# Kernel tuning notes

Hardware: AMD Instinct MI355X
Metric: run time of the kernel (lower is better)

The kernel has to match this reference:

```python
import jax, jax.numpy as jnp
import numpy as np


def setup_inputs() -> dict:
    key = jax.random.key(0)
    k1, k2 = jax.random.split(key)
    B, EMB, CODES, NUM_TOKENS = 16, 64, 16384, 1024
    x_in = jax.random.normal(k1, (B, EMB, CODES), dtype=jnp.float32)
    code_embedding = jax.random.uniform(k2, (NUM_TOKENS, EMB), dtype=jnp.float32)
    return {"x_in": x_in, "code_embedding": code_embedding}


def reference(x_in, code_embedding):
    # x_in: [B, emb, codes]; code_embedding: [num_tokens, emb]
    x_t = jnp.transpose(x_in, (0, 2, 1))  # [B, codes, emb]
    # squared euclidean distances (argmin is invariant to sqrt used by cdist)
    x2 = jnp.sum(x_t * x_t, axis=-1)                      # [B, codes]
    e2 = jnp.sum(code_embedding * code_embedding, axis=-1)  # [num_tokens]
    dots = jnp.einsum('bce,ke->bck', x_t, code_embedding)   # [B, codes, num_tokens]
    dist2 = x2[:, :, None] - 2.0 * dots + e2[None, None, :]
    indices = jnp.argmin(dist2, axis=2)                   # [B, codes]
    x_out = jnp.transpose(code_embedding[indices], (0, 2, 1))  # [B, emb, codes]
    return x_out, indices[:, :, None]  # indices keepdim like torch argmin(keepdim=True)
```

## Files before the change

### kernel.cpp

```cpp
#include <hip/hip_runtime.h>


#define BB 16
#define EMB 64
#define CODES 16384
#define NT 1024
#define NTILES 64

typedef __attribute__((ext_vector_type(8))) short s16x8;
typedef __attribute__((ext_vector_type(4))) float f32x4;
typedef __attribute__((ext_vector_type(4))) int i32x4;
typedef unsigned int u32;

__device__ inline short bf16_hi(float f) { return (short)(__builtin_bit_cast(u32, f) >> 16); }
__device__ inline float hi_part(float f) { return __builtin_bit_cast(float, __builtin_bit_cast(u32, f) & 0xFFFF0000u); }
__device__ inline u32 umin_(u32 a, u32 b) { return a < b ? a : b; }
__device__ inline u32 umax_(u32 a, u32 b) { return a > b ? a : b; }

#define WSE_OFF   0
#define WSH_OFF   266240
#define WSH2_OFF  270336

__global__ __launch_bounds__(256) void vq_prep(const float* __restrict__ E,
                                               char* __restrict__ wsE,
                                               float* __restrict__ wsh,
                                               float* __restrict__ wsh2) {
  const int bid = blockIdx.x, tid = threadIdx.x;
  if (bid < 32) {
    const int gid = bid * 256 + tid;
    const int nt = gid >> 7, ks = (gid >> 6) & 1, lane = gid & 63;
    const int col = lane & 15, quad = lane >> 4;
    const int n = nt * 16 + col;
    const int k0 = ks * 32 + quad * 8;
    const float* ep = E + n * EMB + k0;
    s16x8 hv, lv;
    #pragma unroll
    for (int j = 0; j < 8; ++j) {
      float v = ep[j];
      float hf = hi_part(v);
      hv[j] = bf16_hi(v);
      lv[j] = bf16_hi(v - hf);
    }
    char* base = wsE + ((size_t)nt << 12) + ((size_t)ks << 10) + lane * 16;
    *(i32x4*)(base)        = __builtin_bit_cast(i32x4, hv);
    *(i32x4*)(base + 2048) = __builtin_bit_cast(i32x4, lv);
  } else {
    const int n = (bid - 32) * 256 + tid;
    if (n < NT) {
      const float4* ep = (const float4*)(E + n * EMB);
      float s = 0.f;
      #pragma unroll
      for (int g = 0; g < 16; ++g) { float4 v = ep[g]; s += v.x*v.x + v.y*v.y + v.z*v.z + v.w*v.w; }
      const float h = -0.5f * s;
      wsh[n] = h;
      wsh2[n] = 16384.f * (h + 128.f);
    }
  }
}

__global__ __launch_bounds__(64, 2) void vq_main(
    const float* __restrict__ x, const float* __restrict__ E,
    const char* __restrict__ wsE, const float* __restrict__ wsh,
    const float* __restrict__ wsh2,
    float* __restrict__ xout, float* __restrict__ iout) {
  __shared__ uint2 cand[64];
  const int lane = threadIdx.x;
  const int col = lane & 15, quad = lane >> 4;
  const int b = blockIdx.y;
  const int c0 = blockIdx.x * 64;

  s16x8 ah[4][2], al[4][2];
  #pragma unroll
  for (int mt = 0; mt < 4; ++mt) {
    #pragma unroll
    for (int ks = 0; ks < 2; ++ks) {
      s16x8 hv, lv;
      #pragma unroll
      for (int j = 0; j < 8; ++j) {
        const int e = ks * 32 + quad * 8 + j;
        float v = x[((size_t)b * EMB + e) * CODES + (size_t)(c0 + mt * 16 + col)] * 16384.f;
        float hf = hi_part(v);
        hv[j] = bf16_hi(v);
        lv[j] = bf16_hi(v - hf);
      }
      ah[mt][ks] = hv;
      al[mt][ks] = lv;
    }
  }

  u32 k1[4][4], k2[4][4];
  #pragma unroll
  for (int mt = 0; mt < 4; ++mt)
    #pragma unroll
    for (int r = 0; r < 4; ++r) { k1[mt][r] = 0u; k2[mt][r] = 0u; }

  u32 inv = 1023u - (u32)col;
  const char* p = wsE + lane * 16;
  const float* hp = wsh2 + col;

  i32x4 nb0 = *(const i32x4*)(p);
  i32x4 nb1 = *(const i32x4*)(p + 1024);
  i32x4 nb2 = *(const i32x4*)(p + 2048);
  i32x4 nb3 = *(const i32x4*)(p + 3072);
  float nch = *hp;

  #pragma unroll 4
  for (int nt = 0; nt < NTILES; ++nt) {
    const s16x8 bh0 = __builtin_bit_cast(s16x8, nb0);
    const s16x8 bh1 = __builtin_bit_cast(s16x8, nb1);
    const s16x8 bl0 = __builtin_bit_cast(s16x8, nb2);
    const s16x8 bl1 = __builtin_bit_cast(s16x8, nb3);
    const float ch = nch;

    p += 4096; hp += 16;
    nb0 = *(const i32x4*)(p);
    nb1 = *(const i32x4*)(p + 1024);
    nb2 = *(const i32x4*)(p + 2048);
    nb3 = *(const i32x4*)(p + 3072);
    nch = *hp;

    f32x4 acc[4];
    #pragma unroll
    for (int mt = 0; mt < 4; ++mt) {
      acc[mt] = (f32x4){ch, ch, ch, ch};
      acc[mt] = __builtin_amdgcn_mfma_f32_16x16x32_bf16(ah[mt][0], bh0, acc[mt], 0, 0, 0);
      acc[mt] = __builtin_amdgcn_mfma_f32_16x16x32_bf16(ah[mt][1], bh1, acc[mt], 0, 0, 0);
      acc[mt] = __builtin_amdgcn_mfma_f32_16x16x32_bf16(al[mt][0], bh0, acc[mt], 0, 0, 0);
      acc[mt] = __builtin_amdgcn_mfma_f32_16x16x32_bf16(al[mt][1], bh1, acc[mt], 0, 0, 0);
      acc[mt] = __builtin_amdgcn_mfma_f32_16x16x32_bf16(ah[mt][0], bl0, acc[mt], 0, 0, 0);
      acc[mt] = __builtin_amdgcn_mfma_f32_16x16x32_bf16(ah[mt][1], bl1, acc[mt], 0, 0, 0);
    }

    #pragma unroll
    for (int mt = 0; mt < 4; ++mt) {
      #pragma unroll
      for (int r = 0; r < 4; ++r) {
        u32 q = (u32)acc[mt][r];
        u32 key = (q << 10) + inv;
        u32 t = umin_(key, k1[mt][r]);
        k1[mt][r] = umax_(key, k1[mt][r]);
        k2[mt][r] = umax_(t, k2[mt][r]);
      }
    }
    inv -= 16u;
  }

  #pragma unroll
  for (int mt = 0; mt < 4; ++mt) {
    #pragma unroll
    for (int r = 0; r < 4; ++r) {
      u32 a1 = k1[mt][r], a2 = k2[mt][r];
      #pragma unroll
      for (int m = 1; m <= 8; m <<= 1) {
        u32 r1 = __shfl_xor(a1, m, 64);
        u32 r2 = __shfl_xor(a2, m, 64);
        u32 t = umin_(a1, r1);
        a1 = umax_(a1, r1);
        a2 = umax_(umax_(a2, r2), t);
      }
      if (col == r) cand[mt * 16 + quad * 4 + r] = make_uint2(a1, a2);
    }
  }
  __syncthreads();

  const u32 K1 = cand[lane].x, K2 = cand[lane].y;
  const int i1 = 1023 - (int)(K1 & 1023u);
  const int i2 = 1023 - (int)(K2 & 1023u);
  const float* xq = x + (size_t)b * EMB * CODES + (size_t)(c0 + lane);
  const float4* e1 = (const float4*)(E + i1 * EMB);
  const float4* e2 = (const float4*)(E + i2 * EMB);
  float d10 = 0, d11 = 0, d12 = 0, d13 = 0, d20 = 0, d21 = 0, d22 = 0, d23 = 0;
  #pragma unroll
  for (int g = 0; g < 16; ++g) {
    float4 a = e1[g], c4 = e2[g];
    float x0 = xq[(size_t)(4 * g + 0) * CODES];
    float x1 = xq[(size_t)(4 * g + 1) * CODES];
    float x2 = xq[(size_t)(4 * g + 2) * CODES];
    float x3 = xq[(size_t)(4 * g + 3) * CODES];
    d10 = fmaf(x0, a.x, d10);  d11 = fmaf(x1, a.y, d11);
    d12 = fmaf(x2, a.z, d12);  d13 = fmaf(x3, a.w, d13);
    d20 = fmaf(x0, c4.x, d20); d21 = fmaf(x1, c4.y, d21);
    d22 = fmaf(x2, c4.z, d22); d23 = fmaf(x3, c4.w, d23);
  }
  const float s1 = ((d10 + d11) + (d12 + d13)) + wsh[i1];
  const float s2 = ((d20 + d21) + (d22 + d23)) + wsh[i2];
  const bool take2 = (s2 > s1) || (s2 == s1 && i2 < i1);
  const int idx = take2 ? i2 : i1;

  const float* Er = E + idx * EMB;
  float* xo = xout + (size_t)b * EMB * CODES + (size_t)(c0 + lane);
  #pragma unroll
  for (int e = 0; e < EMB; ++e) xo[(size_t)e * CODES] = Er[e];
  iout[(size_t)b * CODES + (size_t)(c0 + lane)] = (float)idx;
}

extern "C" void kernel_launch(void* const* d_in, const int* in_sizes, int n_in,
                              void* d_out, int out_size, void* d_ws, size_t ws_size,
                              hipStream_t stream) {
  const float* x = (const float*)d_in[0];
  const float* E = (const float*)d_in[1];
  float* xout = (float*)d_out;
  float* iout = (float*)d_out + (size_t)BB * EMB * CODES;

  char* wsE  = (char*)d_ws + WSE_OFF;
  float* wsh  = (float*)((char*)d_ws + WSH_OFF);
  float* wsh2 = (float*)((char*)d_ws + WSH2_OFF);

  vq_prep<<<36, 256, 0, stream>>>(E, wsE, wsh, wsh2);
  vq_main<<<dim3(CODES / 64, BB), 64, 0, stream>>>(x, E, wsE, wsh, wsh2, xout, iout);
}
```

Before: 225.8 us.

## Stage codebook tiles in double-buffered LDS shared by four waves per block

Blocks grow from one wave covering 64 codes to four waves covering 128 codes, each wave now holding 32 codes. The bf16 hi/lo codebook is loaded cooperatively into double-buffered shared memory in chunks of four tiles, so every wave reuses one staged copy instead of streaming the whole codebook from global memory itself. The final gather and write-out is spread across all 256 threads. The cost is fewer MFMA tiles per wave per codebook fetch, more LDS reads, and a block barrier after every chunk.

```diff
diff --git a/kernel.cpp b/kernel.cpp
--- a/kernel.cpp
+++ b/kernel.cpp
@@ -6,6 +6,8 @@
 #define CODES 16384
 #define NT 1024
 #define NTILES 64
+#define CHUNK 4
+#define EPOCHS (NTILES / CHUNK)
 
 typedef __attribute__((ext_vector_type(8))) short s16x8;
 typedef __attribute__((ext_vector_type(4))) float f32x4;
@@ -58,27 +60,29 @@
   }
 }
 
-__global__ __launch_bounds__(64, 2) void vq_main(
+__global__ __launch_bounds__(256, 5) void vq_main(
     const float* __restrict__ x, const float* __restrict__ E,
     const char* __restrict__ wsE, const float* __restrict__ wsh,
     const float* __restrict__ wsh2,
     float* __restrict__ xout, float* __restrict__ iout) {
-  __shared__ uint2 cand[64];
-  const int lane = threadIdx.x;
+  __shared__ char smem[2 * CHUNK * 4096];
+  const int tid = threadIdx.x;
+  const int wave = tid >> 6, lane = tid & 63;
   const int col = lane & 15, quad = lane >> 4;
   const int b = blockIdx.y;
-  const int c0 = blockIdx.x * 64;
-
-  s16x8 ah[4][2], al[4][2];
+  const int c0 = blockIdx.x * 128;
+  const int cw = c0 + wave * 32;
+
+  s16x8 ah[2][2], al[2][2];
   #pragma unroll
-  for (int mt = 0; mt < 4; ++mt) {
+  for (int mt = 0; mt < 2; ++mt) {
     #pragma unroll
     for (int ks = 0; ks < 2; ++ks) {
       s16x8 hv, lv;
       #pragma unroll
       for (int j = 0; j < 8; ++j) {
         const int e = ks * 32 + quad * 8 + j;
-        float v = x[((size_t)b * EMB + e) * CODES + (size_t)(c0 + mt * 16 + col)] * 16384.f;
+        float v = x[((size_t)b * EMB + e) * CODES + (size_t)(cw + mt * 16 + col)] * 16384.f;
         float hf = hi_part(v);
         hv[j] = bf16_hi(v);
         lv[j] = bf16_hi(v - hf);
@@ -88,65 +92,91 @@
     }
   }
 
-  u32 k1[4][4], k2[4][4];
+  u32 k1[2][4], k2[2][4];
   #pragma unroll
-  for (int mt = 0; mt < 4; ++mt)
+  for (int mt = 0; mt < 2; ++mt)
     #pragma unroll
     for (int r = 0; r < 4; ++r) { k1[mt][r] = 0u; k2[mt][r] = 0u; }
 
   u32 inv = 1023u - (u32)col;
-  const char* p = wsE + lane * 16;
   const float* hp = wsh2 + col;
 
-  i32x4 nb0 = *(const i32x4*)(p);
-  i32x4 nb1 = *(const i32x4*)(p + 1024);
-  i32x4 nb2 = *(const i32x4*)(p + 2048);
-  i32x4 nb3 = *(const i32x4*)(p + 3072);
-  float nch = *hp;
-
-  #pragma unroll 4
-  for (int nt = 0; nt < NTILES; ++nt) {
-    const s16x8 bh0 = __builtin_bit_cast(s16x8, nb0);
-    const s16x8 bh1 = __builtin_bit_cast(s16x8, nb1);
-    const s16x8 bl0 = __builtin_bit_cast(s16x8, nb2);
-    const s16x8 bl1 = __builtin_bit_cast(s16x8, nb3);
-    const float ch = nch;
-
-    p += 4096; hp += 16;
-    nb0 = *(const i32x4*)(p);
-    nb1 = *(const i32x4*)(p + 1024);
-    nb2 = *(const i32x4*)(p + 2048);
-    nb3 = *(const i32x4*)(p + 3072);
-    nch = *hp;
-
-    f32x4 acc[4];
-    #pragma unroll
-    for (int mt = 0; mt < 4; ++mt) {
-      acc[mt] = (f32x4){ch, ch, ch, ch};
-      acc[mt] = __builtin_amdgcn_mfma_f32_16x16x32_bf16(ah[mt][0], bh0, acc[mt], 0, 0, 0);
-      acc[mt] = __builtin_amdgcn_mfma_f32_16x16x32_bf16(ah[mt][1], bh1, acc[mt], 0, 0, 0);
-      acc[mt] = __builtin_amdgcn_mfma_f32_16x16x32_bf16(al[mt][0], bh0, acc[mt], 0, 0, 0);
-      acc[mt] = __builtin_amdgcn_mfma_f32_16x16x32_bf16(al[mt][1], bh1, acc[mt], 0, 0, 0);
-      acc[mt] = __builtin_amdgcn_mfma_f32_16x16x32_bf16(ah[mt][0], bl0, acc[mt], 0, 0, 0);
-      acc[mt] = __builtin_amdgcn_mfma_f32_16x16x32_bf16(ah[mt][1], bl1, acc[mt], 0, 0, 0);
-    }
-
-    #pragma unroll
-    for (int mt = 0; mt < 4; ++mt) {
-      #pragma unroll
-      for (int r = 0; r < 4; ++r) {
-        u32 q = (u32)acc[mt][r];
-        u32 key = (q << 10) + inv;
-        u32 t = umin_(key, k1[mt][r]);
-        k1[mt][r] = umax_(key, k1[mt][r]);
-        k2[mt][r] = umax_(t, k2[mt][r]);
-      }
-    }
-    inv -= 16u;
-  }
-
+  const char* gbase = wsE + wave * 4096 + lane * 16;
+  i32x4 st0, st1, st2, st3;
+  {
+    const char* g = gbase;
+    st0 = *(const i32x4*)(g);
+    st1 = *(const i32x4*)(g + 1024);
+    st2 = *(const i32x4*)(g + 2048);
+    st3 = *(const i32x4*)(g + 3072);
+    char* d = smem + wave * 4096 + lane * 16;
+    *(i32x4*)(d)        = st0;
+    *(i32x4*)(d + 1024) = st1;
+    *(i32x4*)(d + 2048) = st2;
+    *(i32x4*)(d + 3072) = st3;
+  }
+  __syncthreads();
+
+  for (int c = 0; c < EPOCHS; ++c) {
+    const char* rb = smem + (c & 1) * (CHUNK * 4096) + lane * 16;
+    char* wb = smem + ((c + 1) & 1) * (CHUNK * 4096) + wave * 4096 + lane * 16;
+
+    if (c < EPOCHS - 1) {
+      const char* g = gbase + (size_t)(c + 1) * (CHUNK * 4096);
+      st0 = *(const i32x4*)(g);
+      st1 = *(const i32x4*)(g + 1024);
+      st2 = *(const i32x4*)(g + 2048);
+      st3 = *(const i32x4*)(g + 3072);
+    }
+
+    #pragma unroll
+    for (int t = 0; t < CHUNK; ++t) {
+      const char* p = rb + t * 4096;
+      const s16x8 bh0 = __builtin_bit_cast(s16x8, *(const i32x4*)(p));
+      const s16x8 bh1 = __builtin_bit_cast(s16x8, *(const i32x4*)(p + 1024));
+      const s16x8 bl0 = __builtin_bit_cast(s16x8, *(const i32x4*)(p + 2048));
+      const s16x8 bl1 = __builtin_bit_cast(s16x8, *(const i32x4*)(p + 3072));
+      const float ch = hp[(c * CHUNK + t) * 16];
+
+      f32x4 acc[2];
+      #pragma unroll
+      for (int mt = 0; mt < 2; ++mt) {
+        acc[mt] = (f32x4){ch, ch, ch, ch};
+        acc[mt] = __builtin_amdgcn_mfma_f32_16x16x32_bf16(ah[mt][0], bh0, acc[mt], 0, 0, 0);
+        acc[mt] = __builtin_amdgcn_mfma_f32_16x16x32_bf16(ah[mt][1], bh1, acc[mt], 0, 0, 0);
+        acc[mt] = __builtin_amdgcn_mfma_f32_16x16x32_bf16(al[mt][0], bh0, acc[mt], 0, 0, 0);
+        acc[mt] = __builtin_amdgcn_mfma_f32_16x16x32_bf16(al[mt][1], bh1, acc[mt], 0, 0, 0);
+        acc[mt] = __builtin_amdgcn_mfma_f32_16x16x32_bf16(ah[mt][0], bl0, acc[mt], 0, 0, 0);
+        acc[mt] = __builtin_amdgcn_mfma_f32_16x16x32_bf16(ah[mt][1], bl1, acc[mt], 0, 0, 0);
+      }
+
+      #pragma unroll
+      for (int mt = 0; mt < 2; ++mt) {
+        #pragma unroll
+        for (int r = 0; r < 4; ++r) {
+          u32 q = (u32)acc[mt][r];
+          u32 key = (q << 10) + inv;
+          u32 tt = umin_(key, k1[mt][r]);
+          k1[mt][r] = umax_(key, k1[mt][r]);
+          k2[mt][r] = umax_(tt, k2[mt][r]);
+        }
+      }
+      inv -= 16u;
+    }
+
+    if (c < EPOCHS - 1) {
+      *(i32x4*)(wb)        = st0;
+      *(i32x4*)(wb + 1024) = st1;
+      *(i32x4*)(wb + 2048) = st2;
+      *(i32x4*)(wb + 3072) = st3;
+    }
+    __syncthreads();
+  }
+
+  uint2* cand = (uint2*)smem;
+  int* idxs = (int*)(smem + 1024);
   #pragma unroll
-  for (int mt = 0; mt < 4; ++mt) {
+  for (int mt = 0; mt < 2; ++mt) {
     #pragma unroll
     for (int r = 0; r < 4; ++r) {
       u32 a1 = k1[mt][r], a2 = k2[mt][r];
@@ -158,40 +188,49 @@
         a1 = umax_(a1, r1);
         a2 = umax_(umax_(a2, r2), t);
       }
-      if (col == r) cand[mt * 16 + quad * 4 + r] = make_uint2(a1, a2);
+      if (col == r) cand[wave * 32 + mt * 16 + quad * 4 + r] = make_uint2(a1, a2);
     }
   }
   __syncthreads();
 
-  const u32 K1 = cand[lane].x, K2 = cand[lane].y;
-  const int i1 = 1023 - (int)(K1 & 1023u);
-  const int i2 = 1023 - (int)(K2 & 1023u);
-  const float* xq = x + (size_t)b * EMB * CODES + (size_t)(c0 + lane);
-  const float4* e1 = (const float4*)(E + i1 * EMB);
-  const float4* e2 = (const float4*)(E + i2 * EMB);
-  float d10 = 0, d11 = 0, d12 = 0, d13 = 0, d20 = 0, d21 = 0, d22 = 0, d23 = 0;
-  #pragma unroll
-  for (int g = 0; g < 16; ++g) {
-    float4 a = e1[g], c4 = e2[g];
-    float x0 = xq[(size_t)(4 * g + 0) * CODES];
-    float x1 = xq[(size_t)(4 * g + 1) * CODES];
-    float x2 = xq[(size_t)(4 * g + 2) * CODES];
-    float x3 = xq[(size_t)(4 * g + 3) * CODES];
-    d10 = fmaf(x0, a.x, d10);  d11 = fmaf(x1, a.y, d11);
-    d12 = fmaf(x2, a.z, d12);  d13 = fmaf(x3, a.w, d13);
-    d20 = fmaf(x0, c4.x, d20); d21 = fmaf(x1, c4.y, d21);
-    d22 = fmaf(x2, c4.z, d22); d23 = fmaf(x3, c4.w, d23);
-  }
-  const float s1 = ((d10 + d11) + (d12 + d13)) + wsh[i1];
-  const float s2 = ((d20 + d21) + (d22 + d23)) + wsh[i2];
-  const bool take2 = (s2 > s1) || (s2 == s1 && i2 < i1);
-  const int idx = take2 ? i2 : i1;
-
-  const float* Er = E + idx * EMB;
-  float* xo = xout + (size_t)b * EMB * CODES + (size_t)(c0 + lane);
-  #pragma unroll
-  for (int e = 0; e < EMB; ++e) xo[(size_t)e * CODES] = Er[e];
-  iout[(size_t)b * CODES + (size_t)(c0 + lane)] = (float)idx;
+  if (tid < 128) {
+    const u32 K1 = cand[tid].x, K2 = cand[tid].y;
+    const int i1 = 1023 - (int)(K1 & 1023u);
+    const int i2 = 1023 - (int)(K2 & 1023u);
+    const float* xq = x + (size_t)b * EMB * CODES + (size_t)(c0 + tid);
+    const float4* e1 = (const float4*)(E + i1 * EMB);
+    const float4* e2 = (const float4*)(E + i2 * EMB);
+    float d10 = 0, d11 = 0, d12 = 0, d13 = 0, d20 = 0, d21 = 0, d22 = 0, d23 = 0;
+    #pragma unroll
+    for (int g = 0; g < 16; ++g) {
+      float4 a = e1[g], c4 = e2[g];
+      float x0 = xq[(size_t)(4 * g + 0) * CODES];
+      float x1 = xq[(size_t)(4 * g + 1) * CODES];
+      float x2 = xq[(size_t)(4 * g + 2) * CODES];
+      float x3 = xq[(size_t)(4 * g + 3) * CODES];
+      d10 = fmaf(x0, a.x, d10);  d11 = fmaf(x1, a.y, d11);
+      d12 = fmaf(x2, a.z, d12);  d13 = fmaf(x3, a.w, d13);
+      d20 = fmaf(x0, c4.x, d20); d21 = fmaf(x1, c4.y, d21);
+      d22 = fmaf(x2, c4.z, d22); d23 = fmaf(x3, c4.w, d23);
+    }
+    const float s1 = ((d10 + d11) + (d12 + d13)) + wsh[i1];
+    const float s2 = ((d20 + d21) + (d22 + d23)) + wsh[i2];
+    const bool take2 = (s2 > s1) || (s2 == s1 && i2 < i1);
+    const int idx = take2 ? i2 : i1;
+    idxs[tid] = idx;
+    iout[(size_t)b * CODES + (size_t)(c0 + tid)] = (float)idx;
+  }
+  __syncthreads();
+
+  {
+    const int q = tid & 127;
+    const int eh = (tid >> 7) * 32;
+    const int idx = idxs[q];
+    const float* Er = E + idx * EMB + eh;
+    float* xo = xout + ((size_t)b * EMB + eh) * CODES + (size_t)(c0 + q);
+    #pragma unroll
+    for (int e = 0; e < 32; ++e) xo[(size_t)e * CODES] = Er[e];
+  }
 }
 
 extern "C" void kernel_launch(void* const* d_in, const int* in_sizes, int n_in,
@@ -207,5 +246,5 @@
   float* wsh2 = (float*)((char*)d_ws + WSH2_OFF);
 
   vq_prep<<<36, 256, 0, stream>>>(E, wsE, wsh, wsh2);
-  vq_main<<<dim3(CODES / 64, BB), 64, 0, stream>>>(x, E, wsE, wsh, wsh2, xout, iout);
+  vq_main<<<dim3(CODES / 128, BB), 256, 0, stream>>>(x, E, wsE, wsh, wsh2, xout, iout);
 }
```

New measurement: 323.5 us. 1.43x slower.
